# Kernel optimization log

Measured on AMD Instinct MI355X. Metric: run time of the kernel, lower is better.

## Reference

```python
import jax, jax.numpy as jnp
import numpy as np

H = 2048          # hidden_size
E = 16            # n_routed_experts
K = 4             # num_experts_per_tok
I = 1408          # moe_intermediate_size
SH_I = 2 * I      # shared experts intermediate (n_shared_experts * moe_intermediate_size)
B, S = 1, 1024


def setup_inputs() -> dict:
    key = jax.random.key(0)
    ks = jax.random.split(key, 9)
    sc_h = 1.0 / np.sqrt(H)
    sc_i = 1.0 / np.sqrt(I)
    return {
        "hidden_states": jax.random.normal(ks[0], (B, S, H), dtype=jnp.float32),
        "w_gate": jax.random.normal(ks[1], (E, H), dtype=jnp.float32) * sc_h,
        "wg": jax.random.normal(ks[2], (E, H, I), dtype=jnp.float32) * sc_h,  # gate_proj per expert
        "wu": jax.random.normal(ks[3], (E, H, I), dtype=jnp.float32) * sc_h,  # up_proj per expert
        "wd": jax.random.normal(ks[4], (E, I, H), dtype=jnp.float32) * sc_i,  # down_proj per expert
        "sg": jax.random.normal(ks[5], (H, SH_I), dtype=jnp.float32) * sc_h,  # shared gate_proj
        "su": jax.random.normal(ks[6], (H, SH_I), dtype=jnp.float32) * sc_h,  # shared up_proj
        "sd": jax.random.normal(ks[7], (SH_I, H), dtype=jnp.float32) * (1.0 / np.sqrt(SH_I)),
    }


def reference(hidden_states, w_gate, wg, wu, wd, sg, su, sd):
    b, s, h = hidden_states.shape
    x = hidden_states.reshape(-1, h)                      # [T, H]
    T = x.shape[0]

    # --- router: softmax (fp32) -> topk -> scatter-add weights into [T, E] ---
    logits = x @ w_gate.T                                 # [T, E]
    probs = jax.nn.softmax(logits.astype(jnp.float32), axis=-1)
    top_w, top_i = jax.lax.top_k(probs, K)                # [T, K]
    routing_weight = jnp.zeros((T, E), dtype=probs.dtype)
    routing_weight = routing_weight.at[jnp.arange(T)[:, None], top_i].add(top_w)  # scatter_add_

    # --- routed experts (grouped SwiGLU MLPs), weighted combine ---
    g = jnp.einsum('th,ehi->tei', x, wg)                  # [T, E, I]
    u = jnp.einsum('th,ehi->tei', x, wu)
    act = jax.nn.silu(g) * u                              # [T, E, I]
    routed = jnp.einsum('te,tei,eih->th', routing_weight, act, wd)  # [T, H]

    # --- shared experts (always on) ---
    shared = (jax.nn.silu(x @ sg) * (x @ su)) @ sd        # [T, H]

    out = (routed + shared).astype(hidden_states.dtype)
    return out.reshape(b, s, h)
```

## Files before the change

### kernel.cpp

```cpp
#include <hip/hip_runtime.h>
#include <hip/hip_bf16.h>
#include <stdint.h>

#define T_NUM 1024
#define H_DIM 2048
#define E_NUM 16
#define TOPK 4
#define I_DIM 1408
#define SHI_DIM 2816

typedef __attribute__((ext_vector_type(4))) float f32x4;
typedef __attribute__((ext_vector_type(8))) short bf16x8;
typedef __attribute__((ext_vector_type(4))) short s16x4;

static __device__ __forceinline__ short f2bf(float f) {
    __hip_bfloat16 h = __float2bfloat16(f);
    return __builtin_bit_cast(short, h);
}
static __device__ __forceinline__ float bf2f(short s) {
    return __bfloat162float(__builtin_bit_cast(__hip_bfloat16, s));
}

__global__ void router_kernel(const float* __restrict__ x, const float* __restrict__ wgate,
                              int* __restrict__ top_e, float* __restrict__ top_w,
                              short* __restrict__ xb) {
    const int t = blockIdx.x;
    const int tid = threadIdx.x;
    __shared__ float xsh[H_DIM];
    const float* xr = x + (size_t)t * H_DIM;
    for (int h = tid; h < H_DIM; h += 256) xsh[h] = xr[h];
    __syncthreads();

    {
        short v[8];
        #pragma unroll
        for (int i = 0; i < 8; ++i) v[i] = f2bf(xsh[tid * 8 + i]);
        *reinterpret_cast<bf16x8*>(xb + (size_t)t * H_DIM + tid * 8) = *(bf16x8*)v;
    }

    const int e = tid >> 4;
    const int j = tid & 15;
    const float* wr = wgate + (size_t)e * H_DIM;
    float acc = 0.f;
    for (int h = j; h < H_DIM; h += 16) acc += xsh[h] * wr[h];
    #pragma unroll
    for (int m = 8; m >= 1; m >>= 1) acc += __shfl_down(acc, m, 16);

    __shared__ float logits[E_NUM];
    if (j == 0) logits[e] = acc;
    __syncthreads();

    if (tid == 0) {
        float mx = logits[0];
        #pragma unroll
        for (int i = 1; i < E_NUM; ++i) mx = fmaxf(mx, logits[i]);
        float p[E_NUM]; float s = 0.f;
        #pragma unroll
        for (int i = 0; i < E_NUM; ++i) { p[i] = expf(logits[i] - mx); s += p[i]; }
        const float inv = 1.f / s;
        #pragma unroll
        for (int i = 0; i < E_NUM; ++i) p[i] *= inv;
        for (int k = 0; k < TOPK; ++k) {
            float best = -1.f; int bi = 0;
            #pragma unroll
            for (int i = 0; i < E_NUM; ++i) if (p[i] > best) { best = p[i]; bi = i; }
            top_e[t * TOPK + k] = bi;
            top_w[t * TOPK + k] = best;
            p[bi] = -2.f;
        }
    }
}

__global__ void perm_kernel(const int* __restrict__ top_e,
                            int* __restrict__ offs, int* __restrict__ perm) {
    __shared__ int cnt[256][E_NUM];
    __shared__ int base[E_NUM];
    const int tid = threadIdx.x;
    int c[E_NUM];
    #pragma unroll
    for (int i = 0; i < E_NUM; ++i) c[i] = 0;
    for (int s = tid * 16; s < tid * 16 + 16; ++s) c[top_e[s]]++;
    #pragma unroll
    for (int i = 0; i < E_NUM; ++i) cnt[tid][i] = c[i];
    __syncthreads();
    if (tid < E_NUM) {
        int run = 0;
        for (int b = 0; b < 256; ++b) { int v = cnt[b][tid]; cnt[b][tid] = run; run += v; }
        base[tid] = run;
    }
    __syncthreads();
    if (tid == 0) {
        int run = 0;
        for (int e2 = 0; e2 < E_NUM; ++e2) { int v = base[e2]; base[e2] = run; offs[e2] = run; run += v; }
        offs[E_NUM] = run;
    }
    __syncthreads();
    int run[E_NUM];
    #pragma unroll
    for (int i = 0; i < E_NUM; ++i) run[i] = base[i] + cnt[tid][i];
    for (int s = tid * 16; s < tid * 16 + 16; ++s) {
        int e2 = top_e[s];
        perm[run[e2]++] = s;
    }
}

__global__ void swiglu_kernel(const short* __restrict__ g, const short* __restrict__ u,
                              short* __restrict__ act, int n8) {
    const int i = blockIdx.x * 256 + threadIdx.x;
    if (i >= n8) return;
    bf16x8 gv = *reinterpret_cast<const bf16x8*>(g + (size_t)i * 8);
    bf16x8 uv = *reinterpret_cast<const bf16x8*>(u + (size_t)i * 8);
    short o[8];
    #pragma unroll
    for (int j = 0; j < 8; ++j) {
        float gf = bf2f(gv[j]);
        float uf = bf2f(uv[j]);
        o[j] = f2bf(gf / (1.f + __expf(-gf)) * uf);
    }
    *reinterpret_cast<bf16x8*>(act + (size_t)i * 8) = *(bf16x8*)o;
}

template<int MODE>
__global__ __launch_bounds__(256, 3) void gemm_nb1(
    const short* __restrict__ A, int lda, int Kdim,
    const float* __restrict__ B1g, const float* __restrict__ B2g, int ldb,
    void* __restrict__ Out1v, void* __restrict__ Out2v, int ldo,
    const int* __restrict__ perm, const int* __restrict__ offs,
    const float* __restrict__ top_w, int nmt, int nnt, int nsplit)
{
    constexpr int KP = 40;
    __shared__ short As[2][128 * KP];
    __shared__ short Bs[2][128 * KP];
    __shared__ int   rows_a[128];
    __shared__ int   rows_o[128];
    __shared__ float w_m[128];

    const int tid = threadIdx.x;

    int wgid = blockIdx.x;
    {
        const int nwg = gridDim.x;
        const int qq = nwg >> 3, rr = nwg & 7;
        const int xcd = wgid & 7, lin = wgid >> 3;
        wgid = (xcd < rr ? xcd * (qq + 1) : rr * (qq + 1) + (xcd - rr) * qq) + lin;
    }
    const int mt  = wgid % nmt;
    const int ntt = (wgid / nmt) % nnt;
    const int e   = wgid / (nmt * nnt);

    int off = 0, cnt = T_NUM;
    const float* B1 = B1g;
    const float* B2 = B2g;
    if constexpr (MODE == 0) {
        off = offs[e]; cnt = offs[e + 1] - off;
        if (mt * 128 >= cnt) return;
        B1 = B1g + (size_t)e * H_DIM * I_DIM;
        B2 = B2g + (size_t)e * H_DIM * I_DIM;
    }
    if constexpr (MODE == 2) {
        off = offs[e]; cnt = offs[e + 1] - off;
        if (mt * 128 >= cnt) return;
        B1 = B1g + (size_t)e * I_DIM * H_DIM;
    }
    const float* Bsel = (ntt < nsplit) ? B1 : B2;
    const int ncol = (ntt % nsplit) * 128;

    if (tid < 128) {
        const int gm = mt * 128 + tid;
        if constexpr (MODE == 0) {
            int s = perm[off + (gm < cnt ? gm : cnt - 1)];
            rows_a[tid] = s >> 2; rows_o[tid] = s; w_m[tid] = 1.f;
        } else if constexpr (MODE == 2) {
            int s = perm[off + (gm < cnt ? gm : cnt - 1)];
            rows_a[tid] = s; rows_o[tid] = s >> 2; w_m[tid] = top_w[s];
        } else {
            rows_a[tid] = gm; rows_o[tid] = gm; w_m[tid] = 1.f;
        }
    }
    __syncthreads();

    int raReg[2];
    #pragma unroll
    for (int it = 0; it < 2; ++it) raReg[it] = rows_a[it * 64 + (tid >> 2)];

    bf16x8 aReg[2];
    float  bReg[4][4];

    auto gload = [&](int kt) {
        const int k0 = kt * 32;
        #pragma unroll
        for (int it = 0; it < 2; ++it) {
            const int q = it * 256 + tid;
            const int ko = (q & 3) * 8;
            aReg[it] = *reinterpret_cast<const bf16x8*>(A + (size_t)raReg[it] * lda + k0 + ko);
        }
        #pragma unroll
        for (int it = 0; it < 4; ++it) {
            const int q = it * 256 + tid;
            const int n = q & 127, kb = (q >> 7) * 4;
            const float* p1 = Bsel + (size_t)(k0 + kb) * ldb + ncol + n;
            #pragma unroll
            for (int dk = 0; dk < 4; ++dk) bReg[it][dk] = p1[(size_t)dk * ldb];
        }
    };

    auto swrite = [&](int buf) {
        #pragma unroll
        for (int it = 0; it < 2; ++it) {
            const int q = it * 256 + tid;
            const int m = q >> 2, ko = (q & 3) * 8;
            *reinterpret_cast<bf16x8*>(&As[buf][m * KP + ko]) = aReg[it];
        }
        #pragma unroll
        for (int it = 0; it < 4; ++it) {
            const int q = it * 256 + tid;
            const int n = q & 127, kb = (q >> 7) * 4;
            s16x4 v = { f2bf(bReg[it][0]), f2bf(bReg[it][1]), f2bf(bReg[it][2]), f2bf(bReg[it][3]) };
            *reinterpret_cast<s16x4*>(&Bs[buf][n * KP + kb]) = v;
        }
    };

    f32x4 acc[4][4];
    #pragma unroll
    for (int i = 0; i < 4; ++i)
        #pragma unroll
        for (int j = 0; j < 4; ++j) acc[i][j] = (f32x4)0.f;

    const int lane = tid & 63;
    const int wr = (tid >> 7), wc = (tid >> 6) & 1;
    const int lrow = lane & 15;
    const int lko = (lane >> 4) * 8;

    auto compute = [&](int buf) {
        bf16x8 af[4];
        #pragma unroll
        for (int mi = 0; mi < 4; ++mi)
            af[mi] = *reinterpret_cast<const bf16x8*>(&As[buf][(wr * 64 + mi * 16 + lrow) * KP + lko]);
        #pragma unroll
        for (int ni = 0; ni < 4; ++ni) {
            bf16x8 bfr = *reinterpret_cast<const bf16x8*>(&Bs[buf][(wc * 64 + ni * 16 + lrow) * KP + lko]);
            #pragma unroll
            for (int mi = 0; mi < 4; ++mi)
                acc[mi][ni] = __builtin_amdgcn_mfma_f32_16x16x32_bf16(af[mi], bfr, acc[mi][ni], 0, 0, 0);
        }
    };

    const int NK = Kdim / 32;
    gload(0);
    int cur = 0;
    for (int kt = 0; kt < NK; ++kt) {
        swrite(cur);
        __syncthreads();
        if (kt + 1 < NK) gload(kt + 1);
        compute(cur);
        cur ^= 1;
    }

    #pragma unroll
    for (int mi = 0; mi < 4; ++mi) {
        #pragma unroll
        for (int j = 0; j < 4; ++j) {
            const int ml = wr * 64 + mi * 16 + (lane >> 4) * 4 + j;
            const int gm = mt * 128 + ml;
            if constexpr (MODE == 0 || MODE == 2) { if (gm >= cnt) continue; }
            const int orow = (MODE == 0 || MODE == 2) ? rows_o[ml] : gm;
            const float wsc = w_m[ml];
            #pragma unroll
            for (int ni = 0; ni < 4; ++ni) {
                const int n = ncol + wc * 64 + ni * 16 + (lane & 15);
                const float v = acc[mi][ni][j];
                if constexpr (MODE == 0 || MODE == 1) {
                    short* o = (short*)((ntt < nsplit) ? Out1v : Out2v);
                    o[(size_t)orow * ldo + n] = f2bf(v);
                } else if constexpr (MODE == 2) {
                    atomicAdd(&((float*)Out1v)[(size_t)orow * ldo + n], v * wsc);
                } else {
                    ((float*)Out1v)[(size_t)orow * ldo + n] = v;
                }
            }
        }
    }
}

extern "C" void kernel_launch(void* const* d_in, const int* in_sizes, int n_in,
                              void* d_out, int out_size, void* d_ws, size_t ws_size,
                              hipStream_t stream) {
    const float* x     = (const float*)d_in[0];
    const float* wgate = (const float*)d_in[1];
    const float* wg    = (const float*)d_in[2];
    const float* wu    = (const float*)d_in[3];
    const float* wd    = (const float*)d_in[4];
    const float* sg    = (const float*)d_in[5];
    const float* su    = (const float*)d_in[6];
    const float* sd    = (const float*)d_in[7];
    float* out = (float*)d_out;

    uintptr_t p = (uintptr_t)d_ws;
    auto alloc = [&](size_t bytes) {
        p = (p + 255) & ~(uintptr_t)255;
        void* r = (void*)p; p += bytes; return r;
    };
    int*   top_e = (int*)alloc((size_t)T_NUM * TOPK * sizeof(int));
    float* top_w = (float*)alloc((size_t)T_NUM * TOPK * sizeof(float));
    int*   offs  = (int*)alloc((E_NUM + 1) * sizeof(int));
    int*   perm  = (int*)alloc((size_t)T_NUM * TOPK * sizeof(int));
    short* xb    = (short*)alloc((size_t)T_NUM * H_DIM * 2);
    short* g_r   = (short*)alloc((size_t)T_NUM * TOPK * I_DIM * 2);
    short* u_r   = (short*)alloc((size_t)T_NUM * TOPK * I_DIM * 2);
    short* act_r = (short*)alloc((size_t)T_NUM * TOPK * I_DIM * 2);
    short* g_s   = (short*)alloc((size_t)T_NUM * SHI_DIM * 2);
    short* u_s   = (short*)alloc((size_t)T_NUM * SHI_DIM * 2);
    short* act_s = (short*)alloc((size_t)T_NUM * SHI_DIM * 2);

    router_kernel<<<T_NUM, 256, 0, stream>>>(x, wgate, top_e, top_w, xb);
    perm_kernel<<<1, 256, 0, stream>>>(top_e, offs, perm);

    const int nmtT = T_NUM / 128;
    const int nnI  = I_DIM / 128;
    const int nnH  = H_DIM / 128;
    const int nnS  = SHI_DIM / 128;

    gemm_nb1<1><<<nmtT * (2 * nnS), 256, 0, stream>>>(
        xb, H_DIM, H_DIM, sg, su, SHI_DIM, g_s, u_s, SHI_DIM,
        nullptr, nullptr, nullptr, nmtT, 2 * nnS, nnS);
    swiglu_kernel<<<(T_NUM * SHI_DIM / 8 + 255) / 256, 256, 0, stream>>>(
        g_s, u_s, act_s, T_NUM * SHI_DIM / 8);
    gemm_nb1<3><<<nmtT * nnH, 256, 0, stream>>>(
        act_s, SHI_DIM, SHI_DIM, sd, nullptr, H_DIM, out, nullptr, H_DIM,
        nullptr, nullptr, nullptr, nmtT, nnH, nnH);

    gemm_nb1<0><<<nmtT * (2 * nnI) * E_NUM, 256, 0, stream>>>(
        xb, H_DIM, H_DIM, wg, wu, I_DIM, g_r, u_r, I_DIM,
        perm, offs, nullptr, nmtT, 2 * nnI, nnI);
    swiglu_kernel<<<(T_NUM * TOPK * I_DIM / 8 + 255) / 256, 256, 0, stream>>>(
        g_r, u_r, act_r, T_NUM * TOPK * I_DIM / 8);
    gemm_nb1<2><<<nmtT * nnH * E_NUM, 256, 0, stream>>>(
        act_r, I_DIM, I_DIM, wd, nullptr, H_DIM, out, nullptr, H_DIM,
        perm, offs, top_w, nmtT, nnH, nnH);
}
```

Measured before the change: 579.2 us.

## Narrow GEMM N-tile to 64 and replace down-proj atomics with bf16 staging plus combine

The GEMM kernel's N tile shrinks from 128 to 64 columns, with occupancy raised to 4 blocks per CU. This doubles the grid and cuts per-block shared memory and accumulator registers. The routed down-projection no longer does fp32 atomicAdd into the output. It writes weighted per-(token,slot) results as bf16 into a scratch buffer, and a new combine kernel sums the four slots into the output. This removes atomic contention at the cost of extra memory traffic, an extra launch, and bf16 rounding of the partial results, while the smaller tile makes each block reuse the A operand less.

```diff
diff --git a/kernel.cpp b/kernel.cpp
--- a/kernel.cpp
+++ b/kernel.cpp
@@ -120,8 +120,29 @@
     *reinterpret_cast<bf16x8*>(act + (size_t)i * 8) = *(bf16x8*)o;
 }
 
+__global__ void combine_kernel(const short* __restrict__ dr, float* __restrict__ out) {
+    const int i = blockIdx.x * 256 + threadIdx.x;
+    const int t = i >> 8;
+    const int h8 = (i & 255) * 8;
+    float s[8];
+    f32x4 o0 = *reinterpret_cast<const f32x4*>(out + (size_t)t * H_DIM + h8);
+    f32x4 o1 = *reinterpret_cast<const f32x4*>(out + (size_t)t * H_DIM + h8 + 4);
+    #pragma unroll
+    for (int j = 0; j < 4; ++j) { s[j] = o0[j]; s[4 + j] = o1[j]; }
+    #pragma unroll
+    for (int k = 0; k < TOPK; ++k) {
+        bf16x8 v = *reinterpret_cast<const bf16x8*>(dr + ((size_t)(t * TOPK + k)) * H_DIM + h8);
+        #pragma unroll
+        for (int j = 0; j < 8; ++j) s[j] += bf2f(v[j]);
+    }
+    f32x4 r0 = { s[0], s[1], s[2], s[3] };
+    f32x4 r1 = { s[4], s[5], s[6], s[7] };
+    *reinterpret_cast<f32x4*>(out + (size_t)t * H_DIM + h8) = r0;
+    *reinterpret_cast<f32x4*>(out + (size_t)t * H_DIM + h8 + 4) = r1;
+}
+
 template<int MODE>
-__global__ __launch_bounds__(256, 3) void gemm_nb1(
+__global__ __launch_bounds__(256, 4) void gemm_n64(
     const short* __restrict__ A, int lda, int Kdim,
     const float* __restrict__ B1g, const float* __restrict__ B2g, int ldb,
     void* __restrict__ Out1v, void* __restrict__ Out2v, int ldo,
@@ -130,7 +151,7 @@
 {
     constexpr int KP = 40;
     __shared__ short As[2][128 * KP];
-    __shared__ short Bs[2][128 * KP];
+    __shared__ short Bs[2][64 * KP];
     __shared__ int   rows_a[128];
     __shared__ int   rows_o[128];
     __shared__ float w_m[128];
@@ -163,7 +184,7 @@
         B1 = B1g + (size_t)e * I_DIM * H_DIM;
     }
     const float* Bsel = (ntt < nsplit) ? B1 : B2;
-    const int ncol = (ntt % nsplit) * 128;
+    const int ncol = (ntt % nsplit) * 64;
 
     if (tid < 128) {
         const int gm = mt * 128 + tid;
@@ -172,7 +193,7 @@
             rows_a[tid] = s >> 2; rows_o[tid] = s; w_m[tid] = 1.f;
         } else if constexpr (MODE == 2) {
             int s = perm[off + (gm < cnt ? gm : cnt - 1)];
-            rows_a[tid] = s; rows_o[tid] = s >> 2; w_m[tid] = top_w[s];
+            rows_a[tid] = s; rows_o[tid] = s; w_m[tid] = top_w[s];
         } else {
             rows_a[tid] = gm; rows_o[tid] = gm; w_m[tid] = 1.f;
         }
@@ -184,7 +205,10 @@
     for (int it = 0; it < 2; ++it) raReg[it] = rows_a[it * 64 + (tid >> 2)];
 
     bf16x8 aReg[2];
-    float  bReg[4][4];
+    float  bReg[8];
+
+    const int bn = tid & 63;
+    const int bkb = (tid >> 6) * 8;
 
     auto gload = [&](int kt) {
         const int k0 = kt * 32;
@@ -194,14 +218,9 @@
             const int ko = (q & 3) * 8;
             aReg[it] = *reinterpret_cast<const bf16x8*>(A + (size_t)raReg[it] * lda + k0 + ko);
         }
-        #pragma unroll
-        for (int it = 0; it < 4; ++it) {
-            const int q = it * 256 + tid;
-            const int n = q & 127, kb = (q >> 7) * 4;
-            const float* p1 = Bsel + (size_t)(k0 + kb) * ldb + ncol + n;
-            #pragma unroll
-            for (int dk = 0; dk < 4; ++dk) bReg[it][dk] = p1[(size_t)dk * ldb];
-        }
+        const float* p1 = Bsel + (size_t)(k0 + bkb) * ldb + ncol + bn;
+        #pragma unroll
+        for (int dk = 0; dk < 8; ++dk) bReg[dk] = p1[(size_t)dk * ldb];
     };
 
     auto swrite = [&](int buf) {
@@ -211,20 +230,17 @@
             const int m = q >> 2, ko = (q & 3) * 8;
             *reinterpret_cast<bf16x8*>(&As[buf][m * KP + ko]) = aReg[it];
         }
-        #pragma unroll
-        for (int it = 0; it < 4; ++it) {
-            const int q = it * 256 + tid;
-            const int n = q & 127, kb = (q >> 7) * 4;
-            s16x4 v = { f2bf(bReg[it][0]), f2bf(bReg[it][1]), f2bf(bReg[it][2]), f2bf(bReg[it][3]) };
-            *reinterpret_cast<s16x4*>(&Bs[buf][n * KP + kb]) = v;
-        }
+        s16x4 v0 = { f2bf(bReg[0]), f2bf(bReg[1]), f2bf(bReg[2]), f2bf(bReg[3]) };
+        s16x4 v1 = { f2bf(bReg[4]), f2bf(bReg[5]), f2bf(bReg[6]), f2bf(bReg[7]) };
+        *reinterpret_cast<s16x4*>(&Bs[buf][bn * KP + bkb]) = v0;
+        *reinterpret_cast<s16x4*>(&Bs[buf][bn * KP + bkb + 4]) = v1;
     };
 
-    f32x4 acc[4][4];
+    f32x4 acc[4][2];
     #pragma unroll
     for (int i = 0; i < 4; ++i)
         #pragma unroll
-        for (int j = 0; j < 4; ++j) acc[i][j] = (f32x4)0.f;
+        for (int j = 0; j < 2; ++j) acc[i][j] = (f32x4)0.f;
 
     const int lane = tid & 63;
     const int wr = (tid >> 7), wc = (tid >> 6) & 1;
@@ -237,8 +253,8 @@
         for (int mi = 0; mi < 4; ++mi)
             af[mi] = *reinterpret_cast<const bf16x8*>(&As[buf][(wr * 64 + mi * 16 + lrow) * KP + lko]);
         #pragma unroll
-        for (int ni = 0; ni < 4; ++ni) {
-            bf16x8 bfr = *reinterpret_cast<const bf16x8*>(&Bs[buf][(wc * 64 + ni * 16 + lrow) * KP + lko]);
+        for (int ni = 0; ni < 2; ++ni) {
+            bf16x8 bfr = *reinterpret_cast<const bf16x8*>(&Bs[buf][(wc * 32 + ni * 16 + lrow) * KP + lko]);
             #pragma unroll
             for (int mi = 0; mi < 4; ++mi)
                 acc[mi][ni] = __builtin_amdgcn_mfma_f32_16x16x32_bf16(af[mi], bfr, acc[mi][ni], 0, 0, 0);
@@ -266,14 +282,14 @@
             const int orow = (MODE == 0 || MODE == 2) ? rows_o[ml] : gm;
             const float wsc = w_m[ml];
             #pragma unroll
-            for (int ni = 0; ni < 4; ++ni) {
-                const int n = ncol + wc * 64 + ni * 16 + (lane & 15);
+            for (int ni = 0; ni < 2; ++ni) {
+                const int n = ncol + wc * 32 + ni * 16 + (lane & 15);
                 const float v = acc[mi][ni][j];
                 if constexpr (MODE == 0 || MODE == 1) {
                     short* o = (short*)((ntt < nsplit) ? Out1v : Out2v);
                     o[(size_t)orow * ldo + n] = f2bf(v);
                 } else if constexpr (MODE == 2) {
-                    atomicAdd(&((float*)Out1v)[(size_t)orow * ldo + n], v * wsc);
+                    ((short*)Out1v)[(size_t)orow * ldo + n] = f2bf(v * wsc);
                 } else {
                     ((float*)Out1v)[(size_t)orow * ldo + n] = v;
                 }
@@ -311,30 +327,32 @@
     short* g_s   = (short*)alloc((size_t)T_NUM * SHI_DIM * 2);
     short* u_s   = (short*)alloc((size_t)T_NUM * SHI_DIM * 2);
     short* act_s = (short*)alloc((size_t)T_NUM * SHI_DIM * 2);
+    short* dr    = (short*)alloc((size_t)T_NUM * TOPK * H_DIM * 2);
 
     router_kernel<<<T_NUM, 256, 0, stream>>>(x, wgate, top_e, top_w, xb);
     perm_kernel<<<1, 256, 0, stream>>>(top_e, offs, perm);
 
     const int nmtT = T_NUM / 128;
-    const int nnI  = I_DIM / 128;
-    const int nnH  = H_DIM / 128;
-    const int nnS  = SHI_DIM / 128;
-
-    gemm_nb1<1><<<nmtT * (2 * nnS), 256, 0, stream>>>(
+    const int nnI  = I_DIM / 64;
+    const int nnH  = H_DIM / 64;
+    const int nnS  = SHI_DIM / 64;
+
+    gemm_n64<1><<<nmtT * (2 * nnS), 256, 0, stream>>>(
         xb, H_DIM, H_DIM, sg, su, SHI_DIM, g_s, u_s, SHI_DIM,
         nullptr, nullptr, nullptr, nmtT, 2 * nnS, nnS);
     swiglu_kernel<<<(T_NUM * SHI_DIM / 8 + 255) / 256, 256, 0, stream>>>(
         g_s, u_s, act_s, T_NUM * SHI_DIM / 8);
-    gemm_nb1<3><<<nmtT * nnH, 256, 0, stream>>>(
+    gemm_n64<3><<<nmtT * nnH, 256, 0, stream>>>(
         act_s, SHI_DIM, SHI_DIM, sd, nullptr, H_DIM, out, nullptr, H_DIM,
         nullptr, nullptr, nullptr, nmtT, nnH, nnH);
 
-    gemm_nb1<0><<<nmtT * (2 * nnI) * E_NUM, 256, 0, stream>>>(
+    gemm_n64<0><<<nmtT * (2 * nnI) * E_NUM, 256, 0, stream>>>(
         xb, H_DIM, H_DIM, wg, wu, I_DIM, g_r, u_r, I_DIM,
         perm, offs, nullptr, nmtT, 2 * nnI, nnI);
     swiglu_kernel<<<(T_NUM * TOPK * I_DIM / 8 + 255) / 256, 256, 0, stream>>>(
         g_r, u_r, act_r, T_NUM * TOPK * I_DIM / 8);
-    gemm_nb1<2><<<nmtT * nnH * E_NUM, 256, 0, stream>>>(
-        act_r, I_DIM, I_DIM, wd, nullptr, H_DIM, out, nullptr, H_DIM,
+    gemm_n64<2><<<nmtT * nnH * E_NUM, 256, 0, stream>>>(
+        act_r, I_DIM, I_DIM, wd, nullptr, H_DIM, dr, nullptr, H_DIM,
         perm, offs, top_w, nmtT, nnH, nnH);
-}
+    combine_kernel<<<T_NUM * H_DIM / 8 / 256, 256, 0, stream>>>(dr, out);
+}
```

Result: no change. 577.5 us (-0.3%).
